# Kernel optimization log

Measured on AMD Instinct MI355X. Metric: run time of the kernel, lower is better.

The kernel has to match this reference:

```python
import jax, jax.numpy as jnp
import numpy as np

E = 1024
H = 16
D = E // H
B = 4
T = 2048


def setup_inputs() -> dict:
    key = jax.random.key(0)
    ks = jax.random.split(key, 12)
    s = 0.02
    inp = {
        "query": jax.random.normal(ks[0], (B, T, E), jnp.float32),
        "key_in": jax.random.normal(ks[1], (B, T, E), jnp.float32),
        "value": jax.random.normal(ks[2], (B, T, E), jnp.float32),
        "mask": jnp.tril(jnp.ones((T, T), jnp.int32))[None, None, :, :],
        "Wq": jax.random.normal(ks[3], (E, E), jnp.float32) * s,
        "bq": jnp.zeros((E,), jnp.float32),
        "Wk": jax.random.normal(ks[4], (E, E), jnp.float32) * s,
        "bk": jnp.zeros((E,), jnp.float32),
        "Wv": jax.random.normal(ks[5], (E, E), jnp.float32) * s,
        "bv": jnp.zeros((E,), jnp.float32),
        "Wo": jax.random.normal(ks[6], (E, E), jnp.float32) * s,
        "bo": jnp.zeros((E,), jnp.float32),
    }
    return inp


def _shape(x):
    # [B, T, E] -> [B, H, T, D]
    return x.reshape(B, -1, H, D).transpose(0, 2, 1, 3)


def reference(query, key_in, value, mask, Wq, bq, Wk, bk, Wv, bv, Wo, bo):
    q = _shape(query @ Wq.T + bq)
    k = _shape(key_in @ Wk.T + bk)
    v = _shape(value @ Wv.T + bv)
    scale = 1.0 / jnp.sqrt(jnp.float32(D))
    # [B, H, Tq, Tk]
    scores = jnp.einsum("bhqd,bhkd->bhqk", q, k) * scale
    scores = jnp.where(mask == 0, jnp.float32(-jnp.inf), scores)
    attn = jax.nn.softmax(scores, axis=-1)
    out = jnp.einsum("bhqk,bhkd->bhqd", attn, v)
    out = out.transpose(0, 2, 1, 3).reshape(B, T, E)
    return out @ Wo.T + bo
```

## Files before the change

kernel.cpp:

```cpp
#include <hip/hip_runtime.h>
#include <hip/hip_bf16.h>
#include <cstdint>

#define BB 4
#define TT 2048
#define EE 1024
#define HH 16
#define DD 64
#define BH (BB*HH)
#define MM (BB*TT)
#define KK 1024
#define KSTR 72
#define VSTR 136
#define LOG2E 1.44269504088896340736f

typedef __attribute__((ext_vector_type(8))) short short8;
typedef __attribute__((ext_vector_type(4))) short short4_;
typedef __attribute__((ext_vector_type(4))) float float4_;
typedef __attribute__((ext_vector_type(4))) ushort ushort4_;

__device__ __forceinline__ ushort f2bf(float v) {
    __hip_bfloat16 h = __float2bfloat16(v);
    return *(ushort*)&h;
}

__global__ __launch_bounds__(256) void cvt_kernel(
    const float* __restrict__ s0, ushort* __restrict__ d0, int n0,
    const float* __restrict__ s1, ushort* __restrict__ d1, int n1,
    const float* __restrict__ s2, ushort* __restrict__ d2, int n2,
    const float* __restrict__ s3, ushort* __restrict__ d3, int n3)
{
    const float* s; ushort* d; int n;
    switch (blockIdx.y) {
        case 0: s = s0; d = d0; n = n0; break;
        case 1: s = s1; d = d1; n = n1; break;
        case 2: s = s2; d = d2; n = n2; break;
        default: s = s3; d = d3; n = n3; break;
    }
    int i = (blockIdx.x * 256 + threadIdx.x) * 4;
    if (i >= n) return;
    float4_ v = *(const float4_*)&s[i];
    ushort4_ o;
#pragma unroll
    for (int j = 0; j < 4; j++) o[j] = f2bf(v[j]);
    *(ushort4_*)&d[i] = o;
}

template<int MODE, bool AF32>
__global__ __launch_bounds__(256, 3) void gemm_nt(
    const void* __restrict__ Ain, const ushort* __restrict__ W,
    const float* __restrict__ bias, void* __restrict__ Cout, float scale)
{
    __shared__ __align__(16) ushort As[128*32];
    __shared__ __align__(16) ushort Bs[128*32];

    const int tid  = threadIdx.x;
    const int wave = tid >> 6;
    const int lane = tid & 63;
    const int l15  = lane & 15;
    const int quad = lane >> 4;
    const int wm   = wave & 1;
    const int wn   = wave >> 1;

    const long rowBase = (long)blockIdx.y * 128;
    const long colBase = (long)blockIdx.x * 128;

    int sr[2], sc[2];
#pragma unroll
    for (int it = 0; it < 2; it++) {
        int idx = it * 256 + tid;
        sr[it] = idx >> 2;
        sc[it] = (idx & 3) * 8;
    }

    short8 pa[2], pw[2];

#pragma unroll
    for (int it = 0; it < 2; it++) {
        if (AF32) {
            const float* Arow = (const float*)Ain + (rowBase + sr[it]) * KK + sc[it];
            float4_ f0 = *(const float4_*)&Arow[0];
            float4_ f1 = *(const float4_*)&Arow[4];
#pragma unroll
            for (int j = 0; j < 4; j++) {
                pa[it][j]     = (short)f2bf(f0[j]);
                pa[it][j + 4] = (short)f2bf(f1[j]);
            }
        } else {
            pa[it] = *(const short8*)((const ushort*)Ain + (rowBase + sr[it]) * KK + sc[it]);
        }
        pw[it] = *(const short8*)&W[(colBase + sr[it]) * KK + sc[it]];
    }

    float4_ acc[4][4];
#pragma unroll
    for (int i = 0; i < 4; i++)
#pragma unroll
        for (int j = 0; j < 4; j++) acc[i][j] = float4_{0.f, 0.f, 0.f, 0.f};

    for (int k0 = 0; k0 < KK; k0 += 32) {
        __syncthreads();
#pragma unroll
        for (int it = 0; it < 2; it++) {
            int idx = it * 256 + tid;
            *(short8*)&As[idx * 8] = pa[it];
            *(short8*)&Bs[idx * 8] = pw[it];
        }
        __syncthreads();

        if (k0 + 32 < KK) {
            const int kn = k0 + 32;
#pragma unroll
            for (int it = 0; it < 2; it++) {
                if (AF32) {
                    const float* Arow = (const float*)Ain + (rowBase + sr[it]) * KK + kn + sc[it];
                    float4_ f0 = *(const float4_*)&Arow[0];
                    float4_ f1 = *(const float4_*)&Arow[4];
#pragma unroll
                    for (int j = 0; j < 4; j++) {
                        pa[it][j]     = (short)f2bf(f0[j]);
                        pa[it][j + 4] = (short)f2bf(f1[j]);
                    }
                } else {
                    pa[it] = *(const short8*)((const ushort*)Ain + (rowBase + sr[it]) * KK + kn + sc[it]);
                }
                pw[it] = *(const short8*)&W[(colBase + sr[it]) * KK + kn + sc[it]];
            }
        }

        short8 af[4], bf[4];
#pragma unroll
        for (int mt = 0; mt < 4; mt++)
            af[mt] = *(const short8*)&As[(wm*64 + mt*16 + l15) * 32 + quad*8];
#pragma unroll
        for (int nt = 0; nt < 4; nt++)
            bf[nt] = *(const short8*)&Bs[(wn*64 + nt*16 + l15) * 32 + quad*8];
#pragma unroll
        for (int mt = 0; mt < 4; mt++)
#pragma unroll
            for (int nt = 0; nt < 4; nt++)
                acc[mt][nt] = __builtin_amdgcn_mfma_f32_16x16x32_bf16(
                    af[mt], bf[nt], acc[mt][nt], 0, 0, 0);
    }

#pragma unroll
    for (int nt = 0; nt < 4; nt++) {
        const long col = colBase + wn*64 + nt*16 + l15;
        const float bv = bias[col];
#pragma unroll
        for (int mt = 0; mt < 4; mt++) {
            const long row0 = rowBase + wm*64 + mt*16 + quad*4;
            if (MODE == 2) {
                const long h = col >> 6, d = col & (DD - 1);
                const long b = row0 >> 11, t0 = row0 & (TT - 1);
                ushort4_ pk;
#pragma unroll
                for (int i = 0; i < 4; i++) pk[i] = f2bf((acc[mt][nt][i] + bv) * scale);
                *(ushort4_*)((ushort*)Cout + ((b*HH + h)*DD + d)*TT + t0) = pk;
            } else {
#pragma unroll
                for (int i = 0; i < 4; i++) {
                    const long row = row0 + i;
                    const float v = (acc[mt][nt][i] + bv) * scale;
                    if (MODE == 0) {
                        ((float*)Cout)[row * EE + col] = v;
                    } else {
                        const long b = row >> 11, t = row & (TT - 1);
                        const long h = col >> 6,  d = col & (DD - 1);
                        ((ushort*)Cout)[(((b*HH + h) * TT) + t) * DD + d] = f2bf(v);
                    }
                }
            }
        }
    }
}

__global__ __launch_bounds__(512, 4) void flash_kernel(
    const ushort* __restrict__ Qh, const ushort* __restrict__ Kh,
    const ushort* __restrict__ Vt, ushort* __restrict__ AO)
{
    __shared__ __align__(16) ushort Ks[128*KSTR];
    __shared__ __align__(16) ushort Vs[64*VSTR];

    const int qt  = (TT/128 - 1) - blockIdx.x;
    const int bh  = blockIdx.y;
    const int tid = threadIdx.x;
    const int wave = tid >> 6, lane = tid & 63;
    const int l15 = lane & 15, quad = lane >> 4;

    const ushort* Qb = Qh + (long)bh * TT * DD;
    const ushort* Kb = Kh + (long)bh * TT * DD;
    const ushort* Vb = Vt + (long)bh * DD * TT;

    const int qrow = qt*128 + wave*16 + l15;
    short8 aq0 = *(const short8*)&Qb[(long)qrow * DD + quad*8];
    short8 aq1 = *(const short8*)&Qb[(long)qrow * DD + 32 + quad*8];

    float4_ o[4];
#pragma unroll
    for (int nt = 0; nt < 4; nt++) o[nt] = float4_{0.f, 0.f, 0.f, 0.f};
    float m_run = -INFINITY, l_run = 0.0f;

    const int nkt = qt + 1;

    short8 kreg[2], vreg[2];
#pragma unroll
    for (int it = 0; it < 2; it++) {
        int c = it * 512 + tid;
        int kk = c >> 3, ks = c & 7;
        kreg[it] = *(const short8*)&Kb[(long)kk * DD + ks*8];
        int dd = c >> 4, vs = c & 15;
        vreg[it] = *(const short8*)&Vb[(long)dd * TT + vs*8];
    }

    for (int kt = 0; kt < nkt; kt++) {
        __syncthreads();
#pragma unroll
        for (int it = 0; it < 2; it++) {
            int c = it * 512 + tid;
            int kk = c >> 3, ks = c & 7;
            *(short8*)&Ks[kk*KSTR + ks*8] = kreg[it];
            int dd = c >> 4, vs = c & 15;
            *(short8*)&Vs[dd*VSTR + vs*8] = vreg[it];
        }
        __syncthreads();

        if (kt + 1 < nkt) {
            const long koff = (long)(kt+1) * 128;
#pragma unroll
            for (int it = 0; it < 2; it++) {
                int c = it * 512 + tid;
                int kk = c >> 3, ks = c & 7;
                kreg[it] = *(const short8*)&Kb[(koff + kk) * DD + ks*8];
                int dd = c >> 4, vs = c & 15;
                vreg[it] = *(const short8*)&Vb[(long)dd * TT + koff + vs*8];
            }
        }

        float4_ s[8];
        __builtin_amdgcn_s_setprio(1);
#pragma unroll
        for (int nt = 0; nt < 8; nt++) {
            short8 bk0 = *(const short8*)&Ks[(nt*16 + l15) * KSTR + quad*8];
            short8 bk1 = *(const short8*)&Ks[(nt*16 + l15) * KSTR + 32 + quad*8];
            float4_ acc = float4_{0.f, 0.f, 0.f, 0.f};
            acc = __builtin_amdgcn_mfma_f32_16x16x32_bf16(bk0, aq0, acc, 0,0,0);
            acc = __builtin_amdgcn_mfma_f32_16x16x32_bf16(bk1, aq1, acc, 0,0,0);
            s[nt] = acc;
        }
        __builtin_amdgcn_s_setprio(0);

        if (kt == nkt - 1) {
#pragma unroll
            for (int nt = 0; nt < 8; nt++) {
#pragma unroll
                for (int i = 0; i < 4; i++) {
                    const int key = kt*128 + nt*16 + quad*4 + i;
                    if (key > qrow) s[nt][i] = -INFINITY;
                }
            }
        }

        float t8[8];
#pragma unroll
        for (int nt = 0; nt < 8; nt++)
            t8[nt] = fmaxf(fmaxf(s[nt][0], s[nt][1]), fmaxf(s[nt][2], s[nt][3]));
        float pm = fmaxf(fmaxf(fmaxf(t8[0], t8[1]), fmaxf(t8[2], t8[3])),
                         fmaxf(fmaxf(t8[4], t8[5]), fmaxf(t8[6], t8[7])));
        pm = fmaxf(pm, __shfl_xor(pm, 16));
        pm = fmaxf(pm, __shfl_xor(pm, 32));

        if (!__all(pm <= m_run + 8.0f)) {
            const float mnew = fmaxf(m_run, pm);
            const float alpha = exp2f(m_run - mnew);
            m_run = mnew;
            l_run *= alpha;
#pragma unroll
            for (int nt = 0; nt < 4; nt++)
#pragma unroll
                for (int i = 0; i < 4; i++) o[nt][i] *= alpha;
        }

        float rs0 = 0.f, rs1 = 0.f, rs2 = 0.f, rs3 = 0.f;
        short8 pb[4];
#pragma unroll
        for (int c = 0; c < 4; c++) {
#pragma unroll
            for (int half = 0; half < 2; half++) {
                const int nt = 2*c + half;
                const float p0 = exp2f(s[nt][0] - m_run);
                const float p1 = exp2f(s[nt][1] - m_run);
                const float p2 = exp2f(s[nt][2] - m_run);
                const float p3 = exp2f(s[nt][3] - m_run);
                rs0 += p0; rs1 += p1; rs2 += p2; rs3 += p3;
                pb[c][half*4 + 0] = (short)f2bf(p0);
                pb[c][half*4 + 1] = (short)f2bf(p1);
                pb[c][half*4 + 2] = (short)f2bf(p2);
                pb[c][half*4 + 3] = (short)f2bf(p3);
            }
        }
        float rs = (rs0 + rs1) + (rs2 + rs3);
        rs += __shfl_xor(rs, 16);
        rs += __shfl_xor(rs, 32);
        l_run += rs;

        __builtin_amdgcn_s_setprio(1);
#pragma unroll
        for (int c = 0; c < 4; c++) {
            const short8 bp = pb[c];
#pragma unroll
            for (int nt = 0; nt < 4; nt++) {
                const ushort* vrow = &Vs[(nt*16 + l15) * VSTR];
                short4_ lo = *(const short4_*)&vrow[(2*c    )*16 + quad*4];
                short4_ hi = *(const short4_*)&vrow[(2*c + 1)*16 + quad*4];
                short8 av;
                av[0]=lo[0]; av[1]=lo[1]; av[2]=lo[2]; av[3]=lo[3];
                av[4]=hi[0]; av[5]=hi[1]; av[6]=hi[2]; av[7]=hi[3];
                o[nt] = __builtin_amdgcn_mfma_f32_16x16x32_bf16(av, bp, o[nt], 0,0,0);
            }
        }
        __builtin_amdgcn_s_setprio(0);
    }

    const int h = bh & (HH - 1);
    const int b = bh >> 4;
    const float inv = 1.0f / l_run;
    const long rowOff = ((long)(b*TT + qrow)) * EE + h*64;
#pragma unroll
    for (int nt = 0; nt < 4; nt++) {
        ushort4_ pk;
#pragma unroll
        for (int i = 0; i < 4; i++) pk[i] = f2bf(o[nt][i] * inv);
        *(ushort4_*)&AO[rowOff + nt*16 + quad*4] = pk;
    }
}

extern "C" void kernel_launch(void* const* d_in, const int* in_sizes, int n_in,
                              void* d_out, int out_size, void* d_ws, size_t ws_size,
                              hipStream_t stream)
{
    const float* query  = (const float*)d_in[0];
    const float* key_in = (const float*)d_in[1];
    const float* value  = (const float*)d_in[2];
    const float* Wq = (const float*)d_in[4];
    const float* bq = (const float*)d_in[5];
    const float* Wk = (const float*)d_in[6];
    const float* bk = (const float*)d_in[7];
    const float* Wv = (const float*)d_in[8];
    const float* bv = (const float*)d_in[9];
    const float* Wo = (const float*)d_in[10];
    const float* bo = (const float*)d_in[11];

    ushort* ws = (ushort*)d_ws;
    const size_t NIN = (size_t)MM * KK;
    const size_t NW  = (size_t)EE * KK;
    ushort* Wqc = ws;
    ushort* Wkc = Wqc + NW;
    ushort* Wvc = Wkc + NW;
    ushort* Woc = Wvc + NW;
    ushort* Qh  = Woc + NW;
    ushort* Kh  = Qh + NIN;
    ushort* Vth = Kh + NIN;
    ushort* AO  = Vth + NIN;

    dim3 gemm_grid(EE/128, MM/128);
    const dim3 cvtW_grid(NW/1024, 4);

    cvt_kernel<<<cvtW_grid, 256, 0, stream>>>(Wq, Wqc, (int)NW, Wk, Wkc, (int)NW,
                                              Wv, Wvc, (int)NW, Wo, Woc, (int)NW);
    gemm_nt<1, true><<<gemm_grid, 256, 0, stream>>>(query,  Wqc, bq, Qh,  0.125f * LOG2E);
    gemm_nt<1, true><<<gemm_grid, 256, 0, stream>>>(key_in, Wkc, bk, Kh,  1.0f);
    gemm_nt<2, true><<<gemm_grid, 256, 0, stream>>>(value,  Wvc, bv, Vth, 1.0f);

    flash_kernel<<<dim3(TT/128, BH), 512, 0, stream>>>(Qh, Kh, Vth, AO);

    gemm_nt<0, false><<<gemm_grid, 256, 0, stream>>>(AO, Woc, bo, d_out, 1.0f);
}
```

Baseline: 438.5 us.

## Batch QKV projections into one launch and load bf16 tiles directly to LDS

Merges the three Q/K/V projection GEMMs into one kernel that picks its operands by blockIdx.z, replacing three launches with one larger grid. Weight tiles, and in the output GEMM both operand tiles, are now loaded with global_load_lds straight into shared memory instead of going through registers. The register prefetch of the next k-tile is dropped for those operands, so their loads are issued after the barrier, which may expose global latency inside the loop.

```diff
diff --git a/kernel.cpp b/kernel.cpp
--- a/kernel.cpp
+++ b/kernel.cpp
@@ -18,6 +18,12 @@
 typedef __attribute__((ext_vector_type(4))) short short4_;
 typedef __attribute__((ext_vector_type(4))) float float4_;
 typedef __attribute__((ext_vector_type(4))) ushort ushort4_;
+
+__device__ __forceinline__ void gl_lds16(const void* g, void* l) {
+    __builtin_amdgcn_global_load_lds(
+        (const __attribute__((address_space(1))) void*)g,
+        (__attribute__((address_space(3))) void*)l, 16, 0, 0);
+}
 
 __device__ __forceinline__ ushort f2bf(float v) {
     __hip_bfloat16 h = __float2bfloat16(v);
@@ -46,13 +52,26 @@
     *(ushort4_*)&d[i] = o;
 }
 
-template<int MODE, bool AF32>
-__global__ __launch_bounds__(256, 3) void gemm_nt(
-    const void* __restrict__ Ain, const ushort* __restrict__ W,
-    const float* __restrict__ bias, void* __restrict__ Cout, float scale)
+__global__ __launch_bounds__(256, 3) void gemm_qkv(
+    const float* __restrict__ Aq, const float* __restrict__ Ak,
+    const float* __restrict__ Av,
+    const ushort* __restrict__ Wqc, const ushort* __restrict__ Wkc,
+    const ushort* __restrict__ Wvc,
+    const float* __restrict__ bq, const float* __restrict__ bk,
+    const float* __restrict__ bv,
+    ushort* __restrict__ Oq, ushort* __restrict__ Ok, ushort* __restrict__ Ov,
+    float qscale)
 {
     __shared__ __align__(16) ushort As[128*32];
     __shared__ __align__(16) ushort Bs[128*32];
+
+    const int z = blockIdx.z;
+    const float*  A    = (z == 0) ? Aq  : (z == 1) ? Ak  : Av;
+    const ushort* W    = (z == 0) ? Wqc : (z == 1) ? Wkc : Wvc;
+    const float*  bias = (z == 0) ? bq  : (z == 1) ? bk  : bv;
+    ushort*       Cout = (z == 0) ? Oq  : (z == 1) ? Ok  : Ov;
+    const float   scale = (z == 0) ? qscale : 1.0f;
+    const bool    modeT = (z == 2);
 
     const int tid  = threadIdx.x;
     const int wave = tid >> 6;
@@ -73,23 +92,17 @@
         sc[it] = (idx & 3) * 8;
     }
 
-    short8 pa[2], pw[2];
-
+    short8 pa[2];
 #pragma unroll
     for (int it = 0; it < 2; it++) {
-        if (AF32) {
-            const float* Arow = (const float*)Ain + (rowBase + sr[it]) * KK + sc[it];
-            float4_ f0 = *(const float4_*)&Arow[0];
-            float4_ f1 = *(const float4_*)&Arow[4];
-#pragma unroll
-            for (int j = 0; j < 4; j++) {
-                pa[it][j]     = (short)f2bf(f0[j]);
-                pa[it][j + 4] = (short)f2bf(f1[j]);
-            }
-        } else {
-            pa[it] = *(const short8*)((const ushort*)Ain + (rowBase + sr[it]) * KK + sc[it]);
-        }
-        pw[it] = *(const short8*)&W[(colBase + sr[it]) * KK + sc[it]];
+        const float* Arow = A + (rowBase + sr[it]) * KK + sc[it];
+        float4_ f0 = *(const float4_*)&Arow[0];
+        float4_ f1 = *(const float4_*)&Arow[4];
+#pragma unroll
+        for (int j = 0; j < 4; j++) {
+            pa[it][j]     = (short)f2bf(f0[j]);
+            pa[it][j + 4] = (short)f2bf(f1[j]);
+        }
     }
 
     float4_ acc[4][4];
@@ -104,7 +117,7 @@
         for (int it = 0; it < 2; it++) {
             int idx = it * 256 + tid;
             *(short8*)&As[idx * 8] = pa[it];
-            *(short8*)&Bs[idx * 8] = pw[it];
+            gl_lds16(W + (colBase + sr[it]) * KK + k0 + sc[it], &Bs[idx * 8]);
         }
         __syncthreads();
 
@@ -112,19 +125,14 @@
             const int kn = k0 + 32;
 #pragma unroll
             for (int it = 0; it < 2; it++) {
-                if (AF32) {
-                    const float* Arow = (const float*)Ain + (rowBase + sr[it]) * KK + kn + sc[it];
-                    float4_ f0 = *(const float4_*)&Arow[0];
-                    float4_ f1 = *(const float4_*)&Arow[4];
-#pragma unroll
-                    for (int j = 0; j < 4; j++) {
-                        pa[it][j]     = (short)f2bf(f0[j]);
-                        pa[it][j + 4] = (short)f2bf(f1[j]);
-                    }
-                } else {
-                    pa[it] = *(const short8*)((const ushort*)Ain + (rowBase + sr[it]) * KK + kn + sc[it]);
+                const float* Arow = A + (rowBase + sr[it]) * KK + kn + sc[it];
+                float4_ f0 = *(const float4_*)&Arow[0];
+                float4_ f1 = *(const float4_*)&Arow[4];
+#pragma unroll
+                for (int j = 0; j < 4; j++) {
+                    pa[it][j]     = (short)f2bf(f0[j]);
+                    pa[it][j + 4] = (short)f2bf(f1[j]);
                 }
-                pw[it] = *(const short8*)&W[(colBase + sr[it]) * KK + kn + sc[it]];
             }
         }
 
@@ -146,31 +154,91 @@
 #pragma unroll
     for (int nt = 0; nt < 4; nt++) {
         const long col = colBase + wn*64 + nt*16 + l15;
-        const float bv = bias[col];
+        const float bvv = bias[col];
+        const long h = col >> 6, d = col & (DD - 1);
 #pragma unroll
         for (int mt = 0; mt < 4; mt++) {
             const long row0 = rowBase + wm*64 + mt*16 + quad*4;
-            if (MODE == 2) {
-                const long h = col >> 6, d = col & (DD - 1);
+            if (modeT) {
                 const long b = row0 >> 11, t0 = row0 & (TT - 1);
                 ushort4_ pk;
 #pragma unroll
-                for (int i = 0; i < 4; i++) pk[i] = f2bf((acc[mt][nt][i] + bv) * scale);
-                *(ushort4_*)((ushort*)Cout + ((b*HH + h)*DD + d)*TT + t0) = pk;
+                for (int i = 0; i < 4; i++) pk[i] = f2bf((acc[mt][nt][i] + bvv) * scale);
+                *(ushort4_*)&Cout[((b*HH + h)*DD + d)*TT + t0] = pk;
             } else {
 #pragma unroll
                 for (int i = 0; i < 4; i++) {
                     const long row = row0 + i;
-                    const float v = (acc[mt][nt][i] + bv) * scale;
-                    if (MODE == 0) {
-                        ((float*)Cout)[row * EE + col] = v;
-                    } else {
-                        const long b = row >> 11, t = row & (TT - 1);
-                        const long h = col >> 6,  d = col & (DD - 1);
-                        ((ushort*)Cout)[(((b*HH + h) * TT) + t) * DD + d] = f2bf(v);
-                    }
+                    const long b = row >> 11, t = row & (TT - 1);
+                    Cout[(((b*HH + h) * TT) + t) * DD + d] =
+                        f2bf((acc[mt][nt][i] + bvv) * scale);
                 }
             }
+        }
+    }
+}
+
+__global__ __launch_bounds__(256, 3) void gemm_out(
+    const ushort* __restrict__ A, const ushort* __restrict__ W,
+    const float* __restrict__ bias, float* __restrict__ Cout)
+{
+    __shared__ __align__(16) ushort As[128*32];
+    __shared__ __align__(16) ushort Bs[128*32];
+
+    const int tid  = threadIdx.x;
+    const int wave = tid >> 6;
+    const int lane = tid & 63;
+    const int l15  = lane & 15;
+    const int quad = lane >> 4;
+    const int wm   = wave & 1;
+    const int wn   = wave >> 1;
+
+    const long rowBase = (long)blockIdx.y * 128;
+    const long colBase = (long)blockIdx.x * 128;
+
+    float4_ acc[4][4];
+#pragma unroll
+    for (int i = 0; i < 4; i++)
+#pragma unroll
+        for (int j = 0; j < 4; j++) acc[i][j] = float4_{0.f, 0.f, 0.f, 0.f};
+
+    for (int k0 = 0; k0 < KK; k0 += 32) {
+        __syncthreads();
+#pragma unroll
+        for (int it = 0; it < 2; it++) {
+            int idx = it * 256 + tid;
+            int r   = idx >> 2;
+            int c8  = (idx & 3) * 8;
+            gl_lds16(A + (rowBase + r) * KK + k0 + c8, &As[idx * 8]);
+            gl_lds16(W + (colBase + r) * KK + k0 + c8, &Bs[idx * 8]);
+        }
+        __syncthreads();
+
+        short8 af[4], bf[4];
+#pragma unroll
+        for (int mt = 0; mt < 4; mt++)
+            af[mt] = *(const short8*)&As[(wm*64 + mt*16 + l15) * 32 + quad*8];
+#pragma unroll
+        for (int nt = 0; nt < 4; nt++)
+            bf[nt] = *(const short8*)&Bs[(wn*64 + nt*16 + l15) * 32 + quad*8];
+#pragma unroll
+        for (int mt = 0; mt < 4; mt++)
+#pragma unroll
+            for (int nt = 0; nt < 4; nt++)
+                acc[mt][nt] = __builtin_amdgcn_mfma_f32_16x16x32_bf16(
+                    af[mt], bf[nt], acc[mt][nt], 0, 0, 0);
+    }
+
+#pragma unroll
+    for (int nt = 0; nt < 4; nt++) {
+        const long col = colBase + wn*64 + nt*16 + l15;
+        const float bv = bias[col];
+#pragma unroll
+        for (int mt = 0; mt < 4; mt++) {
+            const long row0 = rowBase + wm*64 + mt*16 + quad*4;
+#pragma unroll
+            for (int i = 0; i < 4; i++)
+                Cout[(row0 + i) * EE + col] = acc[mt][nt][i] + bv;
         }
     }
 }
@@ -363,16 +431,16 @@
     ushort* Vth = Kh + NIN;
     ushort* AO  = Vth + NIN;
 
-    dim3 gemm_grid(EE/128, MM/128);
     const dim3 cvtW_grid(NW/1024, 4);
 
     cvt_kernel<<<cvtW_grid, 256, 0, stream>>>(Wq, Wqc, (int)NW, Wk, Wkc, (int)NW,
                                               Wv, Wvc, (int)NW, Wo, Woc, (int)NW);
-    gemm_nt<1, true><<<gemm_grid, 256, 0, stream>>>(query,  Wqc, bq, Qh,  0.125f * LOG2E);
-    gemm_nt<1, true><<<gemm_grid, 256, 0, stream>>>(key_in, Wkc, bk, Kh,  1.0f);
-    gemm_nt<2, true><<<gemm_grid, 256, 0, stream>>>(value,  Wvc, bv, Vth, 1.0f);
+
+    gemm_qkv<<<dim3(EE/128, MM/128, 3), 256, 0, stream>>>(
+        query, key_in, value, Wqc, Wkc, Wvc, bq, bk, bv, Qh, Kh, Vth,
+        0.125f * LOG2E);
 
     flash_kernel<<<dim3(TT/128, BH), 512, 0, stream>>>(Qh, Kh, Vth, AO);
 
-    gemm_nt<0, false><<<gemm_grid, 256, 0, stream>>>(AO, Woc, bo, d_out, 1.0f);
-}
+    gemm_out<<<dim3(EE/128, MM/128), 256, 0, stream>>>(AO, Woc, bo, (float*)d_out);
+}
```

New measurement: 432.9 us. No clear change (-1.3%).
